# Kernel optimization log

Hardware: AMD Instinct MI355X
Metric: run time of the kernel (lower is better)

Reference implementation:

```python
import jax, jax.numpy as jnp
import numpy as np

NHEAD = 8
LAYER_NAMES = ('self', 'cross', 'self', 'cross')
EPS = 1e-6


def ln(x, g, b, eps=1e-5):
    m = jnp.mean(x, -1, keepdims=True)
    v = jnp.mean((x - m) ** 2, -1, keepdims=True)
    return (x - m) * jax.lax.rsqrt(v + eps) * g + b


def linear_attention(q, k, v, q_mask, kv_mask):
    # q: [N, L, H, D], k/v: [N, S, H, D]; LoFTR LinearAttention (elu+1 feature map)
    Q = jax.nn.elu(q) + 1.0
    K = jax.nn.elu(k) + 1.0
    if q_mask is not None:
        Q = Q * q_mask[:, :, None, None].astype(Q.dtype)
    if kv_mask is not None:
        mk = kv_mask[:, :, None, None].astype(K.dtype)
        K = K * mk
        v = v * mk
    v_len = v.shape[1]
    v = v / v_len
    KV = jnp.einsum('nshd,nshv->nhdv', K, v)
    Z = 1.0 / (jnp.einsum('nlhd,nhd->nlh', Q, K.sum(1)) + EPS)
    return jnp.einsum('nlhd,nhdv,nlh->nlhv', Q, KV, Z) * v_len


def enc_layer(x, src, q_mask, kv_mask, Wq, Wk, Wv, Wm, W1, W2, g1, b1, g2, b2):
    # x: [N, L, C], src: [N, S, C]
    N, L, C = x.shape
    S = src.shape[1]
    H, D = NHEAD, C // NHEAD
    q = (x @ Wq).reshape(N, L, H, D)
    k = (src @ Wk).reshape(N, S, H, D)
    v = (src @ Wv).reshape(N, S, H, D)
    msg = linear_attention(q, k, v, q_mask, kv_mask).reshape(N, L, C)
    msg = ln(msg @ Wm, g1, b1)
    msg = ln(jnp.tanh(jnp.concatenate([x, msg], axis=-1) @ W1) @ W2, g2, b2)
    return x + msg


def sample_descriptors(kp, fmap, s):
    # kp: [B, L, K, 2] (x, y) raw-image pixel coords; fmap: [B, C, H, W]; s: stride
    B, C, H, W = fmap.shape
    k = kp - s / 2 + 0.5
    denom = jnp.array([W * s - s / 2 - 0.5, H * s - s / 2 - 0.5], dtype=kp.dtype)
    k = (k / denom) * 2.0 - 1.0  # normalized [-1, 1]
    px = (k[..., 0] + 1.0) * 0.5 * (W - 1)  # align_corners=True grid_sample
    py = (k[..., 1] + 1.0) * 0.5 * (H - 1)
    x0 = jnp.floor(px)
    y0 = jnp.floor(py)
    wx = (px - x0)[..., None]
    wy = (py - y0)[..., None]
    x0i = jnp.clip(x0, 0, W - 1).astype(jnp.int32)
    x1i = jnp.clip(x0 + 1, 0, W - 1).astype(jnp.int32)
    y0i = jnp.clip(y0, 0, H - 1).astype(jnp.int32)
    y1i = jnp.clip(y0 + 1, 0, H - 1).astype(jnp.int32)
    fm = jnp.transpose(fmap, (0, 2, 3, 1))  # [B, H, W, C]
    bidx = jnp.arange(B)[:, None, None]
    g00 = fm[bidx, y0i, x0i]
    g01 = fm[bidx, y0i, x1i]
    g10 = fm[bidx, y1i, x0i]
    g11 = fm[bidx, y1i, x1i]
    out = (1 - wy) * ((1 - wx) * g00 + wx * g01) + wy * ((1 - wx) * g10 + wx * g11)
    # SuperPoint-style L2 normalization of sampled descriptors
    out = out / (jnp.linalg.norm(out, axis=-1, keepdims=True) + 1e-8)
    return out  # [B, L, K, C]


def geo_transformer(feat0, feat1, kp0_cross, kp1_cross, mask_self0, mask_self1,
                    mask_cross0, mask_cross1, Wq, Wk, Wv, Wm, W1, W2, g1, b1, g2, b2,
                    h0, w0, h1, w1, scale):
    B, L0, C = feat0.shape
    L1 = feat1.shape[1]
    K = kp0_cross.shape[2]
    for i, name in enumerate(LAYER_NAMES):
        p = (Wq[i], Wk[i], Wv[i], Wm[i], W1[i], W2[i], g1[i], b1[i], g2[i], b2[i])
        if name == 'self':
            # source = masked subset of x == full source with kv-mask (v_length cancels)
            feat0 = enc_layer(feat0, feat0, None, mask_self0, *p)
            feat1 = enc_layer(feat1, feat1, None, mask_self1, *p)
        else:
            fmap0 = jnp.transpose(feat0.reshape(B, h0, w0, C), (0, 3, 1, 2))
            fmap1 = jnp.transpose(feat1.reshape(B, h1, w1, C), (0, 3, 1, 2))
            f0c = sample_descriptors(kp0_cross, fmap0, scale)  # [B, L1, K, C]
            f1c = sample_descriptors(kp1_cross, fmap1, scale)  # [B, L0, K, C]
            x0 = feat0.reshape(B * L0, 1, C)
            x1 = feat1.reshape(B * L1, 1, C)
            nf0 = enc_layer(x0, f1c.reshape(B * L0, K, C), None,
                            mask_cross1.reshape(B * L0, K), *p)
            nf1 = enc_layer(x1, f0c.reshape(B * L1, K, C), None,
                            mask_cross0.reshape(B * L1, K), *p)
            feat0 = nf0.reshape(B, L0, C)
            feat1 = nf1.reshape(B, L1, C)
    return feat0, feat1


def setup_inputs() -> dict:
    key = jax.random.key(0)
    B, H0, W0, C, K, S, NL = 2, 64, 64, 256, 9, 8, 4
    L = H0 * W0
    ks = jax.random.split(key, 16)
    std = (2.0 / (C + C)) ** 0.5
    std2 = (2.0 / (2 * C + 2 * C)) ** 0.5
    std3 = (2.0 / (2 * C + C)) ** 0.5
    kp0 = jnp.stack([
        jax.random.uniform(ks[2], (B, L, K)) * (W0 * S),
        jax.random.uniform(ks[3], (B, L, K)) * (H0 * S)], axis=-1)
    kp1 = jnp.stack([
        jax.random.uniform(ks[4], (B, L, K)) * (W0 * S),
        jax.random.uniform(ks[5], (B, L, K)) * (H0 * S)], axis=-1)
    return {
        'feat0': jax.random.normal(ks[0], (B, L, C), jnp.float32),
        'feat1': jax.random.normal(ks[1], (B, L, C), jnp.float32),
        'kp0_cross': kp0.astype(jnp.float32),
        'kp1_cross': kp1.astype(jnp.float32),
        'mask_self0': jax.random.bernoulli(ks[6], 0.9, (B, L)),
        'mask_self1': jax.random.bernoulli(ks[7], 0.9, (B, L)),
        'mask_cross0': jax.random.bernoulli(ks[8], 0.8, (B, L, K)),
        'mask_cross1': jax.random.bernoulli(ks[9], 0.8, (B, L, K)),
        'Wq': jax.random.normal(ks[10], (NL, C, C), jnp.float32) * std,
        'Wk': jax.random.normal(ks[11], (NL, C, C), jnp.float32) * std,
        'Wv': jax.random.normal(ks[12], (NL, C, C), jnp.float32) * std,
        'Wm': jax.random.normal(ks[13], (NL, C, C), jnp.float32) * std,
        'W1': jax.random.normal(ks[14], (NL, 2 * C, 2 * C), jnp.float32) * std2,
        'W2': jax.random.normal(ks[15], (NL, 2 * C, C), jnp.float32) * std3,
        'g1': jnp.ones((NL, C), jnp.float32),
        'b1': jnp.zeros((NL, C), jnp.float32),
        'g2': jnp.ones((NL, C), jnp.float32),
        'b2': jnp.zeros((NL, C), jnp.float32),
        'h0': H0, 'w0': W0, 'h1': H0, 'w1': W0, 'scale': S,
    }


def reference(feat0, feat1, kp0_cross, kp1_cross, mask_self0, mask_self1,
              mask_cross0, mask_cross1, Wq, Wk, Wv, Wm, W1, W2, g1, b1, g2, b2,
              h0, w0, h1, w1, scale):
    return geo_transformer(feat0, feat1, kp0_cross, kp1_cross, mask_self0, mask_self1,
                           mask_cross0, mask_cross1, Wq, Wk, Wv, Wm, W1, W2,
                           g1, b1, g2, b2, h0, w0, h1, w1, scale)
```

## Files before the change

### kernel.cpp

```cpp
#include <hip/hip_runtime.h>
#include <cstddef>


#define NROWS 16384

typedef unsigned short ushort_t;
typedef __attribute__((ext_vector_type(8))) short short8;
typedef __attribute__((ext_vector_type(4))) float f32x4;
typedef __attribute__((ext_vector_type(4))) unsigned short ushort4_t;
typedef __attribute__((ext_vector_type(8))) unsigned short ushort8_t;
typedef _Float16 half_t;
typedef __attribute__((ext_vector_type(4))) _Float16 half4;
typedef __attribute__((ext_vector_type(8))) _Float16 half8;

__device__ __forceinline__ float b2f(unsigned short u) {
    union { unsigned int i; float f; } v; v.i = (unsigned int)u << 16; return v.f;
}
__device__ __forceinline__ unsigned short f2b(float x) {
    union { float f; unsigned int i; } v; v.f = x;
    unsigned int r = v.i + 0x7fffu + ((v.i >> 16) & 1u);
    return (unsigned short)(r >> 16);
}
__device__ __forceinline__ ushort_t f2h(float x) {
    union { half_t h; ushort_t u; } v; v.h = (half_t)x; return v.u;
}
__device__ __forceinline__ float elu1(float x) {
    return x > 0.f ? x + 1.f : __expf(x);
}

#define ASYNC_COPY16(gptr, lptr) \
    __builtin_amdgcn_global_load_lds((const __attribute__((address_space(1))) void*)(gptr), \
                                     (__attribute__((address_space(3))) void*)(lptr), 16, 0, 0)

__global__ __launch_bounds__(256) void gemm_bf16_kernel(
    const ushort_t* __restrict__ A0, int lda0,
    const ushort_t* __restrict__ Wt, int ldw,
    ushort_t* __restrict__ C, int ldc, int Kd,
    float* __restrict__ zbuf, int znf4)
{
    __shared__ ushort_t As[128 * 64];
    __shared__ ushort_t Bs[128 * 64];

    int tid = threadIdx.x;
    int m0 = blockIdx.y * 128;
    int n0 = blockIdx.x * 128;
    int lane = tid & 63, w = tid >> 6;
    int wrow = w >> 1, wcol = w & 1;
    int quad = lane >> 4, l16 = lane & 15;

    if (zbuf && blockIdx.y == 0) {
        int nblk = gridDim.x;
        for (int i = blockIdx.x * 256 + tid; i < znf4; i += nblk * 256)
            *(float4*)&zbuf[(size_t)i * 4] = (float4){0.f, 0.f, 0.f, 0.f};
    }

    f32x4 acc[4][4];
    #pragma unroll
    for (int i = 0; i < 4; i++)
        #pragma unroll
        for (int j = 0; j < 4; j++) acc[i][j] = (f32x4){0.f, 0.f, 0.f, 0.f};

    for (int kb = 0; kb < Kd; kb += 64) {
        #pragma unroll
        for (int q = 0; q < 4; q++) {
            int s = q * 256 + tid;
            int kk = s >> 9, p = s & 511;
            int row = p >> 2, c4 = p & 3;
            ASYNC_COPY16(A0 + (size_t)(m0 + row) * lda0 + kb + kk * 32 + c4 * 8,
                         (char*)As + s * 16);
        }
        #pragma unroll
        for (int q = 0; q < 4; q++) {
            int s = q * 256 + tid;
            int kk = s >> 9, p = s & 511;
            int row = p >> 2, c4 = p & 3;
            ASYNC_COPY16(Wt + (size_t)(n0 + row) * ldw + kb + kk * 32 + c4 * 8,
                         (char*)Bs + s * 16);
        }
        __syncthreads();

        #pragma unroll
        for (int kk = 0; kk < 2; kk++) {
            short8 af[4], bf[4];
            #pragma unroll
            for (int mt = 0; mt < 4; mt++)
                af[mt] = *(const short8*)&As[kk * 4096 + (wrow * 64 + mt * 16 + l16) * 32 + quad * 8];
            #pragma unroll
            for (int nt = 0; nt < 4; nt++)
                bf[nt] = *(const short8*)&Bs[kk * 4096 + (wcol * 64 + nt * 16 + l16) * 32 + quad * 8];
            #pragma unroll
            for (int mt = 0; mt < 4; mt++)
                #pragma unroll
                for (int nt = 0; nt < 4; nt++)
                    acc[mt][nt] = __builtin_amdgcn_mfma_f32_16x16x32_bf16(
                        af[mt], bf[nt], acc[mt][nt], 0, 0, 0);
        }
        __syncthreads();
    }

    #pragma unroll
    for (int mt = 0; mt < 4; mt++) {
        int row = m0 + wrow * 64 + mt * 16 + quad * 4;
        #pragma unroll
        for (int nt = 0; nt < 4; nt++) {
            int col = n0 + wcol * 64 + nt * 16 + l16;
            #pragma unroll
            for (int r = 0; r < 4; r++)
                C[(size_t)(row + r) * ldc + col] = f2h(acc[mt][nt][r]);
        }
    }
}

__global__ __launch_bounds__(256) void mlp_ln_fused_kernel(
    const ushort_t* __restrict__ MSG, const ushort_t* __restrict__ Wmt,
    const float* __restrict__ g1, const float* __restrict__ b1,
    const ushort_t* __restrict__ Xb,
    const ushort_t* __restrict__ W1t, const ushort_t* __restrict__ W2t,
    const float* __restrict__ g2, const float* __restrict__ bp,
    ushort_t* __restrict__ XbfOut, const float* __restrict__ Xin,
    float* __restrict__ Xout)
{
    __shared__ ushort_t XB[32 * 256];
    __shared__ ushort_t L1s[32 * 256];
    __shared__ ushort_t Tnp[32 * 128];
    __shared__ ushort_t Bs[256 * 64];
    __shared__ ushort_t As[32 * 64];
    __shared__ float stats[256];

    int tid = threadIdx.x;
    int m0 = blockIdx.x * 32;
    int lane = tid & 63, w = tid >> 6;
    int quad = lane >> 4, l16 = lane & 15;

    #pragma unroll
    for (int i = 0; i < 4; i++) {
        int s = i * 256 + tid;
        int row = s >> 5, gp = s & 31;
        int gsrc = gp ^ (row & 7);
        ASYNC_COPY16(Xb + (size_t)(m0 + row) * 256 + gsrc * 8,
                     (char*)XB + s * 16);
    }

    f32x4 accA[2][4];
    #pragma unroll
    for (int i = 0; i < 2; i++)
        #pragma unroll
        for (int j = 0; j < 4; j++) accA[i][j] = (f32x4){0.f, 0.f, 0.f, 0.f};

    for (int kb = 0; kb < 256; kb += 64) {
        {
            int s = tid;
            int kk = s >> 7, p = s & 127;
            ASYNC_COPY16(MSG + (size_t)(m0 + (p >> 2)) * 256 + kb + kk * 32 + (p & 3) * 8,
                         (char*)As + s * 16);
        }
        #pragma unroll
        for (int q = 0; q < 8; q++) {
            int s = q * 256 + tid;
            int kk = s >> 10, p = s & 1023;
            ASYNC_COPY16(Wmt + (size_t)(p >> 2) * 256 + kb + kk * 32 + (p & 3) * 8,
                         (char*)Bs + s * 16);
        }
        __syncthreads();

        #pragma unroll
        for (int kk = 0; kk < 2; kk++) {
            short8 af[2], bf[4];
            #pragma unroll
            for (int mt = 0; mt < 2; mt++)
                af[mt] = *(const short8*)&As[kk * 1024 + (mt * 16 + l16) * 32 + quad * 8];
            #pragma unroll
            for (int nt = 0; nt < 4; nt++)
                bf[nt] = *(const short8*)&Bs[kk * 8192 + (w * 64 + nt * 16 + l16) * 32 + quad * 8];
            #pragma unroll
            for (int mt = 0; mt < 2; mt++)
                #pragma unroll
                for (int nt = 0; nt < 4; nt++)
                    accA[mt][nt] = __builtin_amdgcn_mfma_f32_16x16x32_bf16(
                        af[mt], bf[nt], accA[mt][nt], 0, 0, 0);
        }
        __syncthreads();
    }

    #pragma unroll
    for (int mt = 0; mt < 2; mt++)
        #pragma unroll
        for (int r = 0; r < 4; r++) {
            float s = 0.f, q = 0.f;
            #pragma unroll
            for (int nt = 0; nt < 4; nt++) {
                float v = accA[mt][nt][r];
                s += v; q += v * v;
            }
            #pragma unroll
            for (int off = 1; off < 16; off <<= 1) {
                s += __shfl_xor(s, off, 64);
                q += __shfl_xor(q, off, 64);
            }
            if (l16 == 0) {
                stats[w * 32 + mt * 16 + quad * 4 + r] = s;
                stats[128 + w * 32 + mt * 16 + quad * 4 + r] = q;
            }
        }
    __syncthreads();

    #pragma unroll
    for (int mt = 0; mt < 2; mt++) {
        #pragma unroll
        for (int r = 0; r < 4; r++) {
            int rl = mt * 16 + quad * 4 + r;
            float s = stats[rl] + stats[32 + rl] + stats[64 + rl] + stats[96 + rl];
            float q = stats[128 + rl] + stats[160 + rl] + stats[192 + rl] + stats[224 + rl];
            float m = s * (1.f / 256.f);
            float var = q * (1.f / 256.f) - m * m;
            float rs = rsqrtf(var + 1e-5f);
            #pragma unroll
            for (int nt = 0; nt < 4; nt++) {
                int col = w * 64 + nt * 16 + l16;
                float y = (accA[mt][nt][r] - m) * rs * g1[col] + b1[col];
                L1s[rl * 256 + (((col >> 3) ^ (rl & 7)) << 3) + (col & 7)] = f2b(y);
            }
        }
    }
    __syncthreads();

    f32x4 acc2[2][2][2];
    #pragma unroll
    for (int a = 0; a < 2; a++)
        #pragma unroll
        for (int i = 0; i < 2; i++)
            #pragma unroll
            for (int j = 0; j < 2; j++) acc2[a][i][j] = (f32x4){0.f, 0.f, 0.f, 0.f};

    #pragma unroll
    for (int np = 0; np < 4; np++) {
        f32x4 acc1[2][2];
        #pragma unroll
        for (int i = 0; i < 2; i++)
            #pragma unroll
            for (int j = 0; j < 2; j++) acc1[i][j] = (f32x4){0.f, 0.f, 0.f, 0.f};

        #pragma unroll
        for (int kb = 0; kb < 512; kb += 128) {
            #pragma unroll
            for (int q = 0; q < 8; q++) {
                int s = q * 256 + tid;
                int kk = s >> 9, p = s & 511;
                ASYNC_COPY16(W1t + (size_t)(np * 128 + (p >> 2)) * 512 + kb + kk * 32 + (p & 3) * 8,
                             (char*)Bs + s * 16);
            }
            __syncthreads();

            #pragma unroll
            for (int kk = 0; kk < 4; kk++) {
                short8 af[2], bfr[2];
                #pragma unroll
                for (int mt = 0; mt < 2; mt++) {
                    int row = mt * 16 + l16;
                    int k = kb + kk * 32 + quad * 8;
                    if (k < 256)
                        af[mt] = *(const short8*)&XB[row * 256 + (((k >> 3) ^ (row & 7)) << 3)];
                    else
                        af[mt] = *(const short8*)&L1s[row * 256 + ((((k - 256) >> 3) ^ (row & 7)) << 3)];
                }
                #pragma unroll
                for (int nt = 0; nt < 2; nt++)
                    bfr[nt] = *(const short8*)&Bs[kk * 4096 + (w * 32 + nt * 16 + l16) * 32 + quad * 8];
                #pragma unroll
                for (int mt = 0; mt < 2; mt++)
                    #pragma unroll
                    for (int nt = 0; nt < 2; nt++)
                        acc1[mt][nt] = __builtin_amdgcn_mfma_f32_16x16x32_bf16(
                            af[mt], bfr[nt], acc1[mt][nt], 0, 0, 0);
            }
            __syncthreads();
        }

        #pragma unroll
        for (int mt = 0; mt < 2; mt++)
            #pragma unroll
            for (int nt = 0; nt < 2; nt++)
                #pragma unroll
                for (int r = 0; r < 4; r++) {
                    int trow = mt * 16 + quad * 4 + r;
                    int c = w * 32 + nt * 16 + l16;
                    Tnp[trow * 128 + (((c >> 3) ^ (trow & 7)) << 3) + (c & 7)] =
                        f2b(tanhf(acc1[mt][nt][r]));
                }
        __syncthreads();

        #pragma unroll
        for (int kb2 = 0; kb2 < 128; kb2 += 64) {
            #pragma unroll
            for (int q = 0; q < 8; q++) {
                int s = q * 256 + tid;
                int kk = s >> 10, p = s & 1023;
                ASYNC_COPY16(W2t + (size_t)(p >> 2) * 512 + np * 128 + kb2 + kk * 32 + (p & 3) * 8,
                             (char*)Bs + s * 16);
            }
            __syncthreads();

            #pragma unroll
            for (int kk = 0; kk < 2; kk++) {
                short8 af[2];
                #pragma unroll
                for (int mt = 0; mt < 2; mt++) {
                    int row = mt * 16 + l16;
                    int klocal = kb2 + kk * 32 + quad * 8;
                    af[mt] = *(const short8*)&Tnp[row * 128 + (((klocal >> 3) ^ (row & 7)) << 3)];
                }
                #pragma unroll
                for (int pass = 0; pass < 2; pass++)
                    #pragma unroll
                    for (int nt = 0; nt < 2; nt++) {
                        short8 bfr = *(const short8*)&Bs[kk * 8192 +
                            (pass * 128 + w * 32 + nt * 16 + l16) * 32 + quad * 8];
                        #pragma unroll
                        for (int mt = 0; mt < 2; mt++)
                            acc2[pass][mt][nt] = __builtin_amdgcn_mfma_f32_16x16x32_bf16(
                                af[mt], bfr, acc2[pass][mt][nt], 0, 0, 0);
                    }
            }
            __syncthreads();
        }
    }

    #pragma unroll
    for (int mt = 0; mt < 2; mt++)
        #pragma unroll
        for (int r = 0; r < 4; r++) {
            float s = 0.f, q = 0.f;
            #pragma unroll
            for (int pass = 0; pass < 2; pass++)
                #pragma unroll
                for (int nt = 0; nt < 2; nt++) {
                    float v = acc2[pass][mt][nt][r];
                    s += v; q += v * v;
                }
            #pragma unroll
            for (int off = 1; off < 16; off <<= 1) {
                s += __shfl_xor(s, off, 64);
                q += __shfl_xor(q, off, 64);
            }
            if (l16 == 0) {
                stats[w * 32 + mt * 16 + quad * 4 + r] = s;
                stats[128 + w * 32 + mt * 16 + quad * 4 + r] = q;
            }
        }
    __syncthreads();

    #pragma unroll
    for (int mt = 0; mt < 2; mt++) {
        #pragma unroll
        for (int r = 0; r < 4; r++) {
            int rl = mt * 16 + quad * 4 + r;
            float s = stats[rl] + stats[32 + rl] + stats[64 + rl] + stats[96 + rl];
            float q = stats[128 + rl] + stats[160 + rl] + stats[192 + rl] + stats[224 + rl];
            float m = s * (1.f / 256.f);
            float var = q * (1.f / 256.f) - m * m;
            float rs = rsqrtf(var + 1e-5f);
            size_t row = (size_t)(m0 + rl);
            #pragma unroll
            for (int pass = 0; pass < 2; pass++)
                #pragma unroll
                for (int nt = 0; nt < 2; nt++) {
                    int col = pass * 128 + w * 32 + nt * 16 + l16;
                    float y = (acc2[pass][mt][nt][r] - m) * rs * g2[col] + bp[col];
                    float xn = Xin[row * 256 + col] + y;
                    Xout[row * 256 + col] = xn;
                    XbfOut[row * 256 + col] = f2b(xn);
                }
        }
    }
}

__global__ __launch_bounds__(256) void wprep_kernel(
    const float* __restrict__ Wq, const float* __restrict__ Wk,
    const float* __restrict__ Wv, const float* __restrict__ Wm,
    const float* __restrict__ W1, const float* __restrict__ W2,
    ushort_t* __restrict__ Wqkvt, ushort_t* __restrict__ Wmt,
    ushort_t* __restrict__ W1t, ushort_t* __restrict__ W2t)
{
    int t = blockIdx.x;
    int layer = t / 640, r = t % 640;
    const float* src; ushort_t* dst;
    int ldsrc, lddst, tn, tk;
    if (r < 192) {
        int grp = r / 64, rr = r % 64; tn = rr / 8; tk = rr % 8;
        src = (grp == 0 ? Wq : grp == 1 ? Wk : Wv) + (size_t)layer * 65536;
        ldsrc = 256;
        dst = Wqkvt + (size_t)layer * 196608 + (size_t)grp * 65536;
        lddst = 256;
    } else if (r < 256) {
        int rr = r - 192; tn = rr / 8; tk = rr % 8;
        src = Wm + (size_t)layer * 65536; ldsrc = 256;
        dst = Wmt + (size_t)layer * 65536; lddst = 256;
    } else if (r < 512) {
        int rr = r - 256; tn = rr / 16; tk = rr % 16;
        src = W1 + (size_t)layer * 262144; ldsrc = 512;
        dst = W1t + (size_t)layer * 262144; lddst = 512;
    } else {
        int rr = r - 512; tn = rr / 16; tk = rr % 16;
        src = W2 + (size_t)layer * 131072; ldsrc = 256;
        dst = W2t + (size_t)layer * 131072; lddst = 512;
    }
    int n0 = tn * 32, k0 = tk * 32;
    __shared__ float tileS[32][33];
    int j = threadIdx.x & 31, i0 = threadIdx.x >> 5;
    #pragma unroll
    for (int p = 0; p < 4; p++) {
        int i = i0 + p * 8;
        tileS[i][j] = src[(size_t)(k0 + i) * ldsrc + n0 + j];
    }
    __syncthreads();
    #pragma unroll
    for (int p = 0; p < 4; p++) {
        int i = i0 + p * 8;
        dst[(size_t)(n0 + i) * lddst + k0 + j] = f2b(tileS[j][i]);
    }
}

__global__ __launch_bounds__(256) void init_kernel(
    const float* __restrict__ f0, const float* __restrict__ f1,
    float* __restrict__ X, ushort_t* __restrict__ Xbf)
{
    int idx = blockIdx.x * 256 + threadIdx.x;
    size_t e = (size_t)idx * 4;
    float4 v = (e < 2097152) ? *(const float4*)&f0[e] : *(const float4*)&f1[e - 2097152];
    *(float4*)&X[e] = v;
    ushort4_t u = { f2b(v.x), f2b(v.y), f2b(v.z), f2b(v.w) };
    *(ushort4_t*)&Xbf[e] = u;
}

__global__ __launch_bounds__(256) void kv_reduce_kernel(
    const ushort_t* __restrict__ QKV,
    const int* __restrict__ mask0, const int* __restrict__ mask1,
    float* __restrict__ KV, float* __restrict__ Ksum)
{
    int g = blockIdx.y;
    int t = g >> 4, b = (g >> 3) & 1, h = g & 7;
    const int* mask = t ? mask1 : mask0;
    int rowbase = t * 8192 + b * 4096;
    int s_begin = blockIdx.x * 256;

    __shared__ float sK[32][32];
    __shared__ float sV[32][32];

    int tid = threadIdx.x;
    int e  = tid & 31;
    int dq = tid >> 5;

    float acc[4] = {0.f, 0.f, 0.f, 0.f};
    float ks[4]  = {0.f, 0.f, 0.f, 0.f};

    for (int s0 = s_begin; s0 < s_begin + 256; s0 += 32) {
        #pragma unroll
        for (int q = 0; q < 2; q++) {
            int idx = tid + q * 256;
            int rl = idx >> 4;
            int part = idx & 15;
            int s = s0 + rl;
            size_t row = (size_t)(rowbase + s);
            float m = mask[b * 4096 + s] ? 1.f : 0.f;
            if (part < 8) {
                half4 u = *(const half4*)&QKV[row * 768 + 256 + h * 32 + part * 4];
                float4 f = { elu1((float)u[0]) * m, elu1((float)u[1]) * m,
                             elu1((float)u[2]) * m, elu1((float)u[3]) * m };
                *(float4*)&sK[rl][part * 4] = f;
            } else {
                half4 u = *(const half4*)&QKV[row * 768 + 512 + h * 32 + (part - 8) * 4];
                float4 f = { (float)u[0] * m, (float)u[1] * m,
                             (float)u[2] * m, (float)u[3] * m };
                *(float4*)&sV[rl][(part - 8) * 4] = f;
            }
        }
        __syncthreads();

        #pragma unroll
        for (int s = 0; s < 32; s++) {
            float4 kq = *(const float4*)&sK[s][dq * 4];
            float vv = sV[s][e];
            acc[0] += kq.x * vv;
            acc[1] += kq.y * vv;
            acc[2] += kq.z * vv;
            acc[3] += kq.w * vv;
            ks[0] += kq.x; ks[1] += kq.y; ks[2] += kq.z; ks[3] += kq.w;
        }
        __syncthreads();
    }

    #pragma unroll
    for (int j = 0; j < 4; j++)
        atomicAdd(&KV[(size_t)g * 1024 + (dq * 4 + j) * 32 + e], acc[j]);
    if (e == 0) {
        #pragma unroll
        for (int j = 0; j < 4; j++)
            atomicAdd(&Ksum[g * 32 + dq * 4 + j], ks[j]);
    }
}

__global__ __launch_bounds__(256) void attn_apply_kernel(
    const ushort_t* __restrict__ QKV, const float* __restrict__ KV,
    const float* __restrict__ Ksum, ushort_t* __restrict__ MSG)
{
    int row = blockIdx.x;
    int t = row >> 13, bb = (row >> 12) & 1;
    int gb = (t * 2 + bb) * 8;
    int c = threadIdx.x, h = c >> 5, e = c & 31;
    int g = gb + h;

    __shared__ float sQ[256];
    float qf = elu1((float)(*(const half_t*)&QKV[(size_t)row * 768 + c]));
    sQ[c] = qf;
    __syncthreads();

    float p = qf * Ksum[g * 32 + e];
    #pragma unroll
    for (int off = 16; off; off >>= 1) p += __shfl_xor(p, off, 32);
    float Z = 1.f / (p + 1e-6f);

    float acc = 0.f;
    #pragma unroll
    for (int d = 0; d < 32; d++)
        acc += sQ[h * 32 + d] * KV[(size_t)g * 1024 + d * 32 + e];

    MSG[(size_t)row * 256 + c] = f2b(acc * Z);
}

__global__ __launch_bounds__(256) void gram_kernel(
    const ushort_t* __restrict__ Xbf, float* __restrict__ Gm)
{
    int a = blockIdx.x * 4 + (threadIdx.x >> 6);
    int lane = threadIdx.x & 63;
    int img = a / 4225;
    int rr = a - img * 4225;
    int ay = rr / 65, ax = rr - ay * 65;
    int xa = ax > 0 ? ax - 1 : 0;
    int xb = ax < 64 ? ax : 63;
    if (ax == 0) xb = 0;
    int ya = ay > 0 ? ay - 1 : 0;
    int yb = ay < 64 ? ay : 63;
    if (ay == 0) yb = 0;

    size_t rbase = (size_t)img * 4096;
    size_t r0 = (rbase + ya * 64 + xa) * 256;
    size_t r1 = (rbase + ya * 64 + xb) * 256;
    size_t r2 = (rbase + yb * 64 + xa) * 256;
    size_t r3 = (rbase + yb * 64 + xb) * 256;

    int c4 = lane * 4;
    ushort4_t u0 = *(const ushort4_t*)&Xbf[r0 + c4];
    ushort4_t u1 = *(const ushort4_t*)&Xbf[r1 + c4];
    ushort4_t u2 = *(const ushort4_t*)&Xbf[r2 + c4];
    ushort4_t u3 = *(const ushort4_t*)&Xbf[r3 + c4];

    float p[10] = {0,0,0,0,0,0,0,0,0,0};
    #pragma unroll
    for (int j = 0; j < 4; j++) {
        float f0 = b2f(u0[j]), f1 = b2f(u1[j]), f2 = b2f(u2[j]), f3 = b2f(u3[j]);
        p[0] += f0 * f0; p[1] += f0 * f1; p[2] += f0 * f2; p[3] += f0 * f3;
        p[4] += f1 * f1; p[5] += f1 * f2; p[6] += f1 * f3;
        p[7] += f2 * f2; p[8] += f2 * f3; p[9] += f3 * f3;
    }
    #pragma unroll
    for (int k = 0; k < 10; k++)
        #pragma unroll
        for (int off = 32; off; off >>= 1) p[k] += __shfl_xor(p[k], off, 64);

    if (lane == 0) {
        #pragma unroll
        for (int k = 0; k < 10; k++) Gm[(size_t)a * 12 + k] = p[k];
    }
}

__global__ __launch_bounds__(256) void cross_fused_kernel(
    const ushort_t* __restrict__ QKV, const float* __restrict__ Gm,
    const float* __restrict__ kp0, const float* __restrict__ kp1,
    const int* __restrict__ maskc0, const int* __restrict__ maskc1,
    ushort_t* __restrict__ MSG)
{
    int wv = threadIdx.x >> 6;
    int lane = threadIdx.x & 63;
    int half = lane >> 5;
    int l32 = lane & 31;

    int blk = blockIdx.x;
    int qd = (blk & 7) >> 1;
    int within = ((blk >> 3) << 1) | (blk & 1);
    int row = qd * 4096 + within * 4 + wv;

    int t = row >> 13;
    int bl = row & 8191;
    int ts = 1 - t;
    const float* kp = ts ? kp1 : kp0;
    const int* mask = (t == 0) ? maskc1 : maskc0;
    int img = ts * 2 + (bl >> 12);
    int rb = img * 4096;
    const float* Gimg = Gm + (size_t)img * 50700;

    int c8 = l32 * 8;

    half8 qu = *(const half8*)&QKV[(size_t)row * 768 + c8];
    float qf[8];
    #pragma unroll
    for (int j = 0; j < 8; j++) qf[j] = elu1((float)qu[j]);

    float mU0, mU1, mU2, mU3, mSm;
    int mPack;
    {
        int msi = l32 % 5;
        int s9 = half + 2 * msi;
        int valid = (s9 < 9);
        int r = bl * 9 + (valid ? s9 : 0);
        mSm = (valid && mask[r] != 0) ? 1.f : 0.f;

        float2 xy = *(const float2*)&kp[(size_t)r * 2];
        float px = (xy.x - 3.5f) * (63.f / 507.5f);
        float py = (xy.y - 3.5f) * (63.f / 507.5f);
        float fx = floorf(px), fy = floorf(py);
        float wx = px - fx, wy = py - fy;
        int ix = (int)fx, iy = (int)fy;
        int xa = ix > 0 ? ix : 0;
        int xb = ix + 1 > 0 ? (ix + 1 < 63 ? ix + 1 : 63) : 0;
        int ya = iy > 0 ? iy : 0;
        int yb = iy + 1 > 0 ? (iy + 1 < 63 ? iy + 1 : 63) : 0;

        float w0 = (1.f - wy) * (1.f - wx);
        float w1 = (1.f - wy) * wx;
        float w2 = wy * (1.f - wx);
        float w3 = wy * wx;

        const float* G = &Gimg[(size_t)((iy + 1) * 65 + (ix + 1)) * 12];
        float4 ga = *(const float4*)&G[0];
        float4 gb4 = *(const float4*)&G[4];
        float2 gc = *(const float2*)&G[8];
        float ss = w0 * w0 * ga.x + w1 * w1 * gb4.x + w2 * w2 * gb4.w + w3 * w3 * gc.y
                 + 2.f * (w0 * w1 * ga.y + w0 * w2 * ga.z + w0 * w3 * ga.w
                        + w1 * w2 * gb4.y + w1 * w3 * gb4.z + w2 * w3 * gc.x);
        float inv = 1.f / (sqrtf(ss) + 1e-8f);
        mU0 = w0 * inv; mU1 = w1 * inv; mU2 = w2 * inv; mU3 = w3 * inv;

        int base = (rb + ya * 64 + xa) * 768;
        mPack = base | (xb - xa) | ((yb - ya) << 1);
    }

    int spack[5];
    float su0[5], su1[5], su2[5], su3[5], sm[5];
    int srcb = half * 32;
    #pragma unroll
    for (int si = 0; si < 5; si++) {
        int src = srcb + si;
        spack[si] = __shfl(mPack, src, 64);
        su0[si] = __shfl(mU0, src, 64);
        su1[si] = __shfl(mU1, src, 64);
        su2[si] = __shfl(mU2, src, 64);
        su3[si] = __shfl(mU3, src, 64);
        sm[si]  = __shfl(mSm, src, 64);
    }

    half8 kR[2][4], vR[2][4];

#define LOADKV(bufi, si_) do { \
        int pk = spack[si_]; \
        int dx = (pk & 1) ? 768 : 0; \
        int dy = (pk & 2) ? 49152 : 0; \
        size_t bK = (size_t)(pk & ~3) + 256 + c8; \
        size_t bV = bK + 256; \
        kR[bufi][0] = *(const half8*)&QKV[bK]; \
        kR[bufi][1] = *(const half8*)&QKV[bK + dx]; \
        kR[bufi][2] = *(const half8*)&QKV[bK + dy]; \
        kR[bufi][3] = *(const half8*)&QKV[bK + dx + dy]; \
        vR[bufi][0] = *(const half8*)&QKV[bV]; \
        vR[bufi][1] = *(const half8*)&QKV[bV + dx]; \
        vR[bufi][2] = *(const half8*)&QKV[bV + dy]; \
        vR[bufi][3] = *(const half8*)&QKV[bV + dx + dy]; \
    } while (0)

    float zsum = 0.f;
    float acc[8] = {0, 0, 0, 0, 0, 0, 0, 0};

    LOADKV(0, 0);
    #pragma unroll
    for (int si = 0; si < 5; si++) {
        int cur = si & 1;
        if (si + 1 < 5) {
            if (cur == 0) LOADKV(1, si + 1);
            else          LOADKV(0, si + 1);
        }
        float u0 = su0[si], u1 = su1[si], u2 = su2[si], u3 = su3[si];
        float p = 0.f;
        #pragma unroll
        for (int j = 0; j < 8; j++) {
            float kc = u0 * (float)kR[cur][0][j] + u1 * (float)kR[cur][1][j]
                     + u2 * (float)kR[cur][2][j] + u3 * (float)kR[cur][3][j];
            p += qf[j] * elu1(kc);
        }
        p += __shfl_xor(p, 1, 64);
        p += __shfl_xor(p, 2, 64);
        p *= sm[si];

        zsum += p;
        float pu0 = p * u0, pu1 = p * u1, pu2 = p * u2, pu3 = p * u3;
        #pragma unroll
        for (int j = 0; j < 8; j++)
            acc[j] += pu0 * (float)vR[cur][0][j] + pu1 * (float)vR[cur][1][j]
                    + pu2 * (float)vR[cur][2][j] + pu3 * (float)vR[cur][3][j];
    }
#undef LOADKV

    zsum += __shfl_xor(zsum, 32, 64);
    #pragma unroll
    for (int j = 0; j < 8; j++) acc[j] += __shfl_xor(acc[j], 32, 64);

    if (half == 0) {
        float Z = 1.f / (zsum + 1e-6f);
        ushort8_t o;
        #pragma unroll
        for (int j = 0; j < 8; j++) o[j] = f2b(acc[j] * Z);
        *(ushort8_t*)&MSG[(size_t)row * 256 + c8] = o;
    }
}


extern "C" void kernel_launch(void* const* d_in, const int* in_sizes, int n_in,
                              void* d_out, int out_size, void* d_ws, size_t ws_size,
                              hipStream_t stream)
{
    const float* feat0 = (const float*)d_in[0];
    const float* feat1 = (const float*)d_in[1];
    const float* kp0 = (const float*)d_in[2];
    const float* kp1 = (const float*)d_in[3];
    const int* ms0 = (const int*)d_in[4];
    const int* ms1 = (const int*)d_in[5];
    const int* mc0 = (const int*)d_in[6];
    const int* mc1 = (const int*)d_in[7];
    const float* Wq = (const float*)d_in[8];
    const float* Wk = (const float*)d_in[9];
    const float* Wv = (const float*)d_in[10];
    const float* Wm = (const float*)d_in[11];
    const float* W1 = (const float*)d_in[12];
    const float* W2 = (const float*)d_in[13];
    const float* g1 = (const float*)d_in[14];
    const float* b1 = (const float*)d_in[15];
    const float* g2 = (const float*)d_in[16];
    const float* b2 = (const float*)d_in[17];

    char* p = (char*)d_ws;
    float*    X     = (float*)p;            p += 16777216;
    ushort_t* Xbf   = (ushort_t*)p;         p += 8388608;
    ushort_t* QKV   = (ushort_t*)p;         p += 25165824;
    ushort_t* MSG   = (ushort_t*)p;         p += 8388608;
    ushort_t* L1bf  = (ushort_t*)p;         p += 8388608;
    float*    KVb   = (float*)p;            p += 131072;
    float*    KSb   = (float*)p;            p += 4096;
    float*    Gm    = (float*)p;            p += 811264;
    ushort_t* Wqkvt = (ushort_t*)p;         p += 1572864;
    ushort_t* Wmt   = (ushort_t*)p;         p += 524288;
    ushort_t* W1t   = (ushort_t*)p;         p += 2097152;
    ushort_t* W2t   = (ushort_t*)p;         p += 1048576;
    (void)L1bf;

    init_kernel<<<4096, 256, 0, stream>>>(feat0, feat1, X, Xbf);
    wprep_kernel<<<2560, 256, 0, stream>>>(Wq, Wk, Wv, Wm, W1, W2, Wqkvt, Wmt, W1t, W2t);

    for (int i = 0; i < 4; i++) {
        const ushort_t* Wqkvt_l = Wqkvt + (size_t)i * 196608;
        const ushort_t* Wmt_l   = Wmt   + (size_t)i * 65536;
        const ushort_t* W1t_l   = W1t   + (size_t)i * 262144;
        const ushort_t* W2t_l   = W2t   + (size_t)i * 131072;
        const float* g1_l = g1 + (size_t)i * 256;
        const float* b1_l = b1 + (size_t)i * 256;
        const float* g2_l = g2 + (size_t)i * 256;
        const float* b2_l = b2 + (size_t)i * 256;
        bool is_self = (i == 0 || i == 2);

        gemm_bf16_kernel<<<dim3(6, 128), 256, 0, stream>>>(
            Xbf, 256, Wqkvt_l, 256, QKV, 768, 256,
            is_self ? KVb : nullptr, 33792 / 4);

        if (is_self) {
            kv_reduce_kernel<<<dim3(16, 32), 256, 0, stream>>>(QKV, ms0, ms1, KVb, KSb);
            attn_apply_kernel<<<NROWS, 256, 0, stream>>>(QKV, KVb, KSb, MSG);
        } else {
            gram_kernel<<<4225, 256, 0, stream>>>(Xbf, Gm);
            cross_fused_kernel<<<NROWS / 4, 256, 0, stream>>>(QKV, Gm, kp0, kp1, mc0, mc1, MSG);
        }

        float* Xout = (i == 3) ? (float*)d_out : X;
        mlp_ln_fused_kernel<<<NROWS / 32, 256, 0, stream>>>(
            MSG, Wmt_l, g1_l, b1_l, Xbf, W1t_l, W2t_l, g2_l, b2_l, Xbf, X, Xout);
    }
}
```

Measured before the change: 563.5 us.

## Pre-tile weight matrices into MFMA fragment order for contiguous B-tile loads

The weight-prep kernel now writes bf16 weights in a blocked layout of 32-wide K chunks and 16-row N groups, with each 16x32 fragment stored contiguously in the order the MFMA B operand reads it. All GEMM kernels (QKV, Wm, W1, W2) load B tiles as contiguous 1KB blocks and index LDS to match. This is meant to make the global-to-LDS async copies fully contiguous and to reduce LDS bank conflicts on the B fragment reads. The cost is a more complex addressing scheme that must stay consistent between the prep kernel and every consumer.

```diff
diff --git a/kernel.cpp b/kernel.cpp
--- a/kernel.cpp
+++ b/kernel.cpp
@@ -32,6 +32,7 @@
     __builtin_amdgcn_global_load_lds((const __attribute__((address_space(1))) void*)(gptr), \
                                      (__attribute__((address_space(3))) void*)(lptr), 16, 0, 0)
 
+
 __global__ __launch_bounds__(256) void gemm_bf16_kernel(
     const ushort_t* __restrict__ A0, int lda0,
     const ushort_t* __restrict__ Wt, int ldw,
@@ -73,8 +74,8 @@
         for (int q = 0; q < 4; q++) {
             int s = q * 256 + tid;
             int kk = s >> 9, p = s & 511;
-            int row = p >> 2, c4 = p & 3;
-            ASYNC_COPY16(Wt + (size_t)(n0 + row) * ldw + kb + kk * 32 + c4 * 8,
+            int rg = p >> 6, gi = p & 63;
+            ASYNC_COPY16(Wt + (((size_t)((kb >> 5) + kk) * 48 + (n0 >> 4) + rg) * 512 + gi * 8),
                          (char*)Bs + s * 16);
         }
         __syncthreads();
@@ -87,7 +88,7 @@
                 af[mt] = *(const short8*)&As[kk * 4096 + (wrow * 64 + mt * 16 + l16) * 32 + quad * 8];
             #pragma unroll
             for (int nt = 0; nt < 4; nt++)
-                bf[nt] = *(const short8*)&Bs[kk * 4096 + (wcol * 64 + nt * 16 + l16) * 32 + quad * 8];
+                bf[nt] = *(const short8*)&Bs[kk * 4096 + (wcol * 4 + nt) * 512 + (quad * 16 + l16) * 8];
             #pragma unroll
             for (int mt = 0; mt < 4; mt++)
                 #pragma unroll
@@ -158,7 +159,8 @@
         for (int q = 0; q < 8; q++) {
             int s = q * 256 + tid;
             int kk = s >> 10, p = s & 1023;
-            ASYNC_COPY16(Wmt + (size_t)(p >> 2) * 256 + kb + kk * 32 + (p & 3) * 8,
+            int rg = p >> 6, gi = p & 63;
+            ASYNC_COPY16(Wmt + (((size_t)((kb >> 5) + kk) * 16 + rg) * 512 + gi * 8),
                          (char*)Bs + s * 16);
         }
         __syncthreads();
@@ -171,7 +173,7 @@
                 af[mt] = *(const short8*)&As[kk * 1024 + (mt * 16 + l16) * 32 + quad * 8];
             #pragma unroll
             for (int nt = 0; nt < 4; nt++)
-                bf[nt] = *(const short8*)&Bs[kk * 8192 + (w * 64 + nt * 16 + l16) * 32 + quad * 8];
+                bf[nt] = *(const short8*)&Bs[kk * 8192 + (w * 4 + nt) * 512 + (quad * 16 + l16) * 8];
             #pragma unroll
             for (int mt = 0; mt < 2; mt++)
                 #pragma unroll
@@ -246,7 +248,8 @@
             for (int q = 0; q < 8; q++) {
                 int s = q * 256 + tid;
                 int kk = s >> 9, p = s & 511;
-                ASYNC_COPY16(W1t + (size_t)(np * 128 + (p >> 2)) * 512 + kb + kk * 32 + (p & 3) * 8,
+                int rg = p >> 6, gi = p & 63;
+                ASYNC_COPY16(W1t + (((size_t)((kb >> 5) + kk) * 32 + np * 8 + rg) * 512 + gi * 8),
                              (char*)Bs + s * 16);
             }
             __syncthreads();
@@ -265,7 +268,7 @@
                 }
                 #pragma unroll
                 for (int nt = 0; nt < 2; nt++)
-                    bfr[nt] = *(const short8*)&Bs[kk * 4096 + (w * 32 + nt * 16 + l16) * 32 + quad * 8];
+                    bfr[nt] = *(const short8*)&Bs[kk * 4096 + (w * 2 + nt) * 512 + (quad * 16 + l16) * 8];
                 #pragma unroll
                 for (int mt = 0; mt < 2; mt++)
                     #pragma unroll
@@ -295,7 +298,8 @@
             for (int q = 0; q < 8; q++) {
                 int s = q * 256 + tid;
                 int kk = s >> 10, p = s & 1023;
-                ASYNC_COPY16(W2t + (size_t)(p >> 2) * 512 + np * 128 + kb2 + kk * 32 + (p & 3) * 8,
+                int rg = p >> 6, gi = p & 63;
+                ASYNC_COPY16(W2t + (((size_t)(np * 4 + (kb2 >> 5) + kk) * 16 + rg) * 512 + gi * 8),
                              (char*)Bs + s * 16);
             }
             __syncthreads();
@@ -314,7 +318,7 @@
                     #pragma unroll
                     for (int nt = 0; nt < 2; nt++) {
                         short8 bfr = *(const short8*)&Bs[kk * 8192 +
-                            (pass * 128 + w * 32 + nt * 16 + l16) * 32 + quad * 8];
+                            (pass * 8 + w * 2 + nt) * 512 + (quad * 16 + l16) * 8];
                         #pragma unroll
                         for (int mt = 0; mt < 2; mt++)
                             acc2[pass][mt][nt] = __builtin_amdgcn_mfma_f32_16x16x32_bf16(
@@ -384,39 +388,42 @@
     int t = blockIdx.x;
     int layer = t / 640, r = t % 640;
     const float* src; ushort_t* dst;
-    int ldsrc, lddst, tn, tk;
+    int ldsrc, tn, tk, n16, nbase;
     if (r < 192) {
         int grp = r / 64, rr = r % 64; tn = rr / 8; tk = rr % 8;
         src = (grp == 0 ? Wq : grp == 1 ? Wk : Wv) + (size_t)layer * 65536;
         ldsrc = 256;
-        dst = Wqkvt + (size_t)layer * 196608 + (size_t)grp * 65536;
-        lddst = 256;
+        dst = Wqkvt + (size_t)layer * 196608;
+        n16 = 48; nbase = grp * 256;
     } else if (r < 256) {
         int rr = r - 192; tn = rr / 8; tk = rr % 8;
         src = Wm + (size_t)layer * 65536; ldsrc = 256;
-        dst = Wmt + (size_t)layer * 65536; lddst = 256;
+        dst = Wmt + (size_t)layer * 65536; n16 = 16; nbase = 0;
     } else if (r < 512) {
         int rr = r - 256; tn = rr / 16; tk = rr % 16;
         src = W1 + (size_t)layer * 262144; ldsrc = 512;
-        dst = W1t + (size_t)layer * 262144; lddst = 512;
+        dst = W1t + (size_t)layer * 262144; n16 = 32; nbase = 0;
     } else {
         int rr = r - 512; tn = rr / 16; tk = rr % 16;
         src = W2 + (size_t)layer * 131072; ldsrc = 256;
-        dst = W2t + (size_t)layer * 131072; lddst = 512;
-    }
-    int n0 = tn * 32, k0 = tk * 32;
+        dst = W2t + (size_t)layer * 131072; n16 = 16; nbase = 0;
+    }
+    int ln0 = tn * 32, k0 = tk * 32;
     __shared__ float tileS[32][33];
     int j = threadIdx.x & 31, i0 = threadIdx.x >> 5;
     #pragma unroll
     for (int p = 0; p < 4; p++) {
         int i = i0 + p * 8;
-        tileS[i][j] = src[(size_t)(k0 + i) * ldsrc + n0 + j];
+        tileS[i][j] = src[(size_t)(k0 + i) * ldsrc + ln0 + j];
     }
     __syncthreads();
     #pragma unroll
     for (int p = 0; p < 4; p++) {
         int i = i0 + p * 8;
-        dst[(size_t)(n0 + i) * lddst + k0 + j] = f2b(tileS[j][i]);
+        int n = nbase + ln0 + i, k = k0 + j;
+        size_t off = ((size_t)(k >> 5) * n16 + (n >> 4)) * 512
+                   + ((k >> 3) & 3) * 128 + (n & 15) * 8 + (k & 7);
+        dst[off] = f2b(tileS[j][i]);
     }
 }
 
```

After: 564.2 us. No clear change (+0.1%).
